# Kernel optimization log

Measured on AMD Instinct MI355X. Metric: run time of the kernel, lower is better.

Reference implementation:

```python
import jax, jax.numpy as jnp
import numpy as np

B, P, T = 64, 8400, 100


def _corners(b):
    # b: [..., 4] in (cx, cy, w, h) -> (x1, y1, x2, y2)
    cx, cy, w, h = b[..., 0], b[..., 1], b[..., 2], b[..., 3]
    return cx - w / 2, cy - h / 2, cx + w / 2, cy + h / 2


def _pairwise_iou(pred_box, tgt_box):
    # pred_box: [B, P, 4], tgt_box: [B, T, 4] -> iou [B, T, P]
    px1, py1, px2, py2 = _corners(pred_box[:, None, :, :])   # [B,1,P]
    tx1, ty1, tx2, ty2 = _corners(tgt_box[:, :, None, :])    # [B,T,1]
    ix1 = jnp.maximum(px1, tx1)
    iy1 = jnp.maximum(py1, ty1)
    ix2 = jnp.minimum(px2, tx2)
    iy2 = jnp.minimum(py2, ty2)
    inter = jnp.maximum(ix2 - ix1, 0.0) * jnp.maximum(iy2 - iy1, 0.0)
    area_p = (px2 - px1) * (py2 - py1)
    area_t = (tx2 - tx1) * (ty2 - ty1)
    return inter / (area_p + area_t - inter + 1e-6)


def setup_inputs() -> dict:
    key = jax.random.key(0)
    k1, k2, k3 = jax.random.split(key, 3)
    predictions = jax.random.uniform(k1, (B, P, 5), dtype=jnp.float32)
    targets = jax.random.uniform(k2, (B, T, 5), dtype=jnp.float32)
    lengths = jax.random.randint(k3, (B,), 0, T, dtype=jnp.int64)
    return {"predictions": predictions, "targets": targets, "lengths": lengths}


def reference(predictions, targets, lengths):
    # predictions: [B, P, 5], targets: [B, T, 5], lengths: [B]
    iou = _pairwise_iou(predictions[..., 1:], targets[..., 1:])  # [B, T, P]
    # strict '>' in original keeps first max; argmax also returns first occurrence
    best_idx = jnp.argmax(iou, axis=-1)                          # [B, T]
    matched = jnp.take_along_axis(predictions, best_idx[..., None], axis=1)  # [B, T, 5]
    sq = jnp.sum((matched - targets) ** 2, axis=-1)              # [B, T]
    valid = jnp.arange(targets.shape[1]) < lengths[:, None]      # [B, T]
    loss = jnp.sum(jnp.where(valid, sq, 0.0)) / predictions.shape[0]
    return loss
```

## Files before the change

### kernel.cpp

```cpp
#include <hip/hip_runtime.h>

#define BB 64
#define PP 8400
#define TT 100
#define TG 5
#define NGRP (TT / TG)

__global__ __launch_bounds__(256) void yolo_match_kernel(
    const float* __restrict__ pred,
    const float* __restrict__ tgt,
    const int*   __restrict__ lengths,
    float* __restrict__ ws)
{
#pragma clang fp contract(off)
    const int blkraw = blockIdx.x;
    const int x    = blkraw & 7;
    const int r    = blkraw >> 3;
    const int bhi  = r / NGRP;
    const int grp  = r - bhi * NGRP;
    const int b    = x + 8 * bhi;
    const int t0   = grp * TG;
    const int tid  = threadIdx.x;

    const float*  pb  = pred + (size_t)b * PP * 5;
    const float4* pb4 = (const float4*)pb;
    const float*  tb  = tgt + ((size_t)b * TT + t0) * 5;

    float tx1[TG], ty1[TG], tx2[TG], ty2[TG], ta[TG];
#pragma unroll
    for (int g = 0; g < TG; ++g) {
        const float tcx = tb[g * 5 + 1], tcy = tb[g * 5 + 2];
        const float tw  = tb[g * 5 + 3], th  = tb[g * 5 + 4];
        tx1[g] = tcx - tw * 0.5f;
        ty1[g] = tcy - th * 0.5f;
        tx2[g] = tcx + tw * 0.5f;
        ty2[g] = tcy + th * 0.5f;
        ta[g]  = (tx2[g] - tx1[g]) * (ty2[g] - ty1[g]);
    }

    float best[TG];
    int   bidx[TG];
#pragma unroll
    for (int g = 0; g < TG; ++g) { best[g] = -1.0f; bidx[g] = 0; }

    for (int g0 = tid; g0 < PP / 4; g0 += 256) {
        const float4 v0 = pb4[g0 * 5 + 0];
        const float4 v1 = pb4[g0 * 5 + 1];
        const float4 v2 = pb4[g0 * 5 + 2];
        const float4 v3 = pb4[g0 * 5 + 3];
        const float4 v4 = pb4[g0 * 5 + 4];
        const float cxs[4] = { v0.y, v1.z, v2.w, v4.x };
        const float cys[4] = { v0.z, v1.w, v3.x, v4.y };
        const float wss[4] = { v0.w, v2.x, v3.y, v4.z };
        const float hss[4] = { v1.x, v2.y, v3.z, v4.w };

#pragma unroll
        for (int j = 0; j < 4; ++j) {
            const float px1 = cxs[j] - wss[j] * 0.5f;
            const float py1 = cys[j] - hss[j] * 0.5f;
            const float px2 = cxs[j] + wss[j] * 0.5f;
            const float py2 = cys[j] + hss[j] * 0.5f;
            const float area_p = (px2 - px1) * (py2 - py1);
            const int   p = g0 * 4 + j;

#pragma unroll
            for (int g = 0; g < TG; ++g) {
                const float ix1 = fmaxf(px1, tx1[g]);
                const float iy1 = fmaxf(py1, ty1[g]);
                const float ix2 = fminf(px2, tx2[g]);
                const float iy2 = fminf(py2, ty2[g]);
                const float inter = fmaxf(ix2 - ix1, 0.0f) * fmaxf(iy2 - iy1, 0.0f);
                const float denom = ((area_p + ta[g]) - inter) + 1e-6f;
                const float iou   = inter / denom;
                if (iou > best[g]) { best[g] = iou; bidx[g] = p; }
            }
        }
    }

    const int lane = tid & 63;
    const int wid  = tid >> 6;
    __shared__ float s_best[4][TG];
    __shared__ int   s_bidx[4][TG];
    __shared__ float s_sq[TG];

#pragma unroll
    for (int g = 0; g < TG; ++g) {
        float bv = best[g];
        int   bi = bidx[g];
        for (int off = 32; off > 0; off >>= 1) {
            const float ob = __shfl_down(bv, off, 64);
            const int   oi = __shfl_down(bi, off, 64);
            if (ob > bv || (ob == bv && oi < bi)) { bv = ob; bi = oi; }
        }
        if (lane == 0) { s_best[wid][g] = bv; s_bidx[wid][g] = bi; }
    }
    __syncthreads();

    if (tid < TG) {
        const int g = tid;
        float bv = s_best[0][g];
        int   bi = s_bidx[0][g];
#pragma unroll
        for (int w = 1; w < 4; ++w) {
            const float ob = s_best[w][g];
            const int   oi = s_bidx[w][g];
            if (ob > bv || (ob == bv && oi < bi)) { bv = ob; bi = oi; }
        }
        const float* mp = pb + bi * 5;
        const float* tp = tb + g * 5;
        float sq = 0.0f;
        for (int k = 0; k < 5; ++k) {
            const float d = mp[k] - tp[k];
            sq += d * d;
        }
        const bool valid = ((t0 + g) < lengths[b]);
        s_sq[g] = valid ? sq : 0.0f;
    }
    __syncthreads();

    if (tid == 0) {
        float s = 0.0f;
#pragma unroll
        for (int g = 0; g < TG; ++g) s += s_sq[g];
        ws[blkraw] = s;
    }
}

__global__ __launch_bounds__(256) void yolo_reduce_kernel(
    const float* __restrict__ ws,
    float* __restrict__ out)
{
    const int tid = threadIdx.x;
    float s = 0.0f;
    for (int i = tid; i < BB * NGRP; i += 256) s += ws[i];

    __shared__ float sm[256];
    sm[tid] = s;
    __syncthreads();
    for (int off = 128; off > 0; off >>= 1) {
        if (tid < off) sm[tid] += sm[tid + off];
        __syncthreads();
    }
    if (tid == 0) out[0] = sm[0] / (float)BB;
}

extern "C" void kernel_launch(void* const* d_in, const int* in_sizes, int n_in,
                              void* d_out, int out_size, void* d_ws, size_t ws_size,
                              hipStream_t stream) {
    const float* pred    = (const float*)d_in[0];
    const float* tgt     = (const float*)d_in[1];
    const int*   lengths = (const int*)d_in[2];
    float* out = (float*)d_out;
    float* ws  = (float*)d_ws;

    yolo_match_kernel<<<BB * NGRP, 256, 0, stream>>>(pred, tgt, lengths, ws);
    yolo_reduce_kernel<<<1, 256, 0, stream>>>(ws, out);
}
```

Measured before the change: 103.5 us.

## Skip IoU divisions via cross-multiplied threshold and fuse final reduction

Each thread now keeps a per-target lower bound on the IoU and computes the division only when inter > bound*denom. The bound is seeded with a block-wide max after the first iteration, so most candidates skip the divide. The two-kernel reduction becomes a last-block-done pattern using an atomic counter, which needs a memset before the kernel. The target group size drops from 5 to 4, creating more blocks. The slightly scaled threshold is meant to keep argmax ties exact, but it adds branch divergence and a __syncthreads inside the loop.

```diff
diff --git a/kernel.cpp b/kernel.cpp
--- a/kernel.cpp
+++ b/kernel.cpp
@@ -3,14 +3,18 @@
 #define BB 64
 #define PP 8400
 #define TT 100
-#define TG 5
+#define TG 4
 #define NGRP (TT / TG)
+#define NBLK (BB * NGRP)
+#define ONE_MEPS 0.99999904632568359375f
 
 __global__ __launch_bounds__(256) void yolo_match_kernel(
     const float* __restrict__ pred,
     const float* __restrict__ tgt,
     const int*   __restrict__ lengths,
-    float* __restrict__ ws)
+    float*       __restrict__ partials,
+    unsigned*    __restrict__ count,
+    float*       __restrict__ out)
 {
 #pragma clang fp contract(off)
     const int blkraw = blockIdx.x;
@@ -21,6 +25,8 @@
     const int b    = x + 8 * bhi;
     const int t0   = grp * TG;
     const int tid  = threadIdx.x;
+    const int lane = tid & 63;
+    const int wid  = tid >> 6;
 
     const float*  pb  = pred + (size_t)b * PP * 5;
     const float4* pb4 = (const float4*)pb;
@@ -40,10 +46,14 @@
 
     float best[TG];
     int   bidx[TG];
+    float barf[TG];
 #pragma unroll
-    for (int g = 0; g < TG; ++g) { best[g] = -1.0f; bidx[g] = 0; }
+    for (int g = 0; g < TG; ++g) { best[g] = -1.0f; bidx[g] = 0; barf[g] = -1.0f; }
 
-    for (int g0 = tid; g0 < PP / 4; g0 += 256) {
+    __shared__ float s_red[4][TG];
+
+    int iter = 0;
+    for (int g0 = tid; g0 < PP / 4; g0 += 256, ++iter) {
         const float4 v0 = pb4[g0 * 5 + 0];
         const float4 v1 = pb4[g0 * 5 + 1];
         const float4 v2 = pb4[g0 * 5 + 2];
@@ -71,14 +81,32 @@
                 const float iy2 = fminf(py2, ty2[g]);
                 const float inter = fmaxf(ix2 - ix1, 0.0f) * fmaxf(iy2 - iy1, 0.0f);
                 const float denom = ((area_p + ta[g]) - inter) + 1e-6f;
-                const float iou   = inter / denom;
-                if (iou > best[g]) { best[g] = iou; bidx[g] = p; }
+                if (__builtin_expect(inter > barf[g] * denom, 0)) {
+                    const float q = inter / denom;
+                    if (q > best[g]) { best[g] = q; bidx[g] = p; }
+                    barf[g] = fmaxf(barf[g], q * ONE_MEPS);
+                }
+            }
+        }
+
+        if (iter == 0) {
+#pragma unroll
+            for (int g = 0; g < TG; ++g) {
+                float bv = best[g];
+                for (int off = 32; off > 0; off >>= 1)
+                    bv = fmaxf(bv, __shfl_down(bv, off, 64));
+                if (lane == 0) s_red[wid][g] = bv;
+            }
+            __syncthreads();
+#pragma unroll
+            for (int g = 0; g < TG; ++g) {
+                const float gb = fmaxf(fmaxf(s_red[0][g], s_red[1][g]),
+                                       fmaxf(s_red[2][g], s_red[3][g]));
+                barf[g] = fmaxf(barf[g], gb * ONE_MEPS);
             }
         }
     }
 
-    const int lane = tid & 63;
-    const int wid  = tid >> 6;
     __shared__ float s_best[4][TG];
     __shared__ int   s_bidx[4][TG];
     __shared__ float s_sq[TG];
@@ -118,30 +146,28 @@
     }
     __syncthreads();
 
+    __shared__ bool amLast;
     if (tid == 0) {
+        partials[blkraw] = s_sq[0] + s_sq[1] + s_sq[2] + s_sq[3];
+        __threadfence();
+        const unsigned old = atomicAdd(count, 1u);
+        amLast = (old == (unsigned)(NBLK - 1));
+    }
+    __syncthreads();
+
+    if (amLast) {
+        __threadfence();
         float s = 0.0f;
-#pragma unroll
-        for (int g = 0; g < TG; ++g) s += s_sq[g];
-        ws[blkraw] = s;
+        for (int i = tid; i < NBLK; i += 256) s += partials[i];
+        __shared__ float sm[256];
+        sm[tid] = s;
+        __syncthreads();
+        for (int off = 128; off > 0; off >>= 1) {
+            if (tid < off) sm[tid] += sm[tid + off];
+            __syncthreads();
+        }
+        if (tid == 0) out[0] = sm[0] / (float)BB;
     }
-}
-
-__global__ __launch_bounds__(256) void yolo_reduce_kernel(
-    const float* __restrict__ ws,
-    float* __restrict__ out)
-{
-    const int tid = threadIdx.x;
-    float s = 0.0f;
-    for (int i = tid; i < BB * NGRP; i += 256) s += ws[i];
-
-    __shared__ float sm[256];
-    sm[tid] = s;
-    __syncthreads();
-    for (int off = 128; off > 0; off >>= 1) {
-        if (tid < off) sm[tid] += sm[tid + off];
-        __syncthreads();
-    }
-    if (tid == 0) out[0] = sm[0] / (float)BB;
 }
 
 extern "C" void kernel_launch(void* const* d_in, const int* in_sizes, int n_in,
@@ -151,8 +177,11 @@
     const float* tgt     = (const float*)d_in[1];
     const int*   lengths = (const int*)d_in[2];
     float* out = (float*)d_out;
-    float* ws  = (float*)d_ws;
 
-    yolo_match_kernel<<<BB * NGRP, 256, 0, stream>>>(pred, tgt, lengths, ws);
-    yolo_reduce_kernel<<<1, 256, 0, stream>>>(ws, out);
+    unsigned* count    = (unsigned*)d_ws;
+    float*    partials = ((float*)d_ws) + 1;
+
+    hipMemsetAsync(count, 0, sizeof(unsigned), stream);
+    yolo_match_kernel<<<NBLK, 256, 0, stream>>>(pred, tgt, lengths,
+                                                partials, count, out);
 }
```

Measured after the change: 122.1 us. 1.18x slower.
